# Optimization experiments

Measured on AMD Instinct MI355X. Metric: run time of the kernel, lower is better.

The kernel has to match this reference:

```python
import jax, jax.numpy as jnp
import numpy as np

B, Q, K, QSIZE, KSIZE, H, VDIM = 4, 1024, 1024, 256, 256, 32, 256


def setup_inputs() -> dict:
    key = jax.random.key(0)
    ks = jax.random.split(key, 10)
    return {
        "keys": jax.random.normal(ks[0], (B, K, KSIZE), dtype=jnp.float32),
        "queries": jax.random.normal(ks[1], (B, Q, QSIZE), dtype=jnp.float32),
        "values": jax.random.normal(ks[2], (B, K, VDIM), dtype=jnp.float32),
        "valid_lens": jax.random.randint(ks[3], (B,), 1, K + 1, dtype=jnp.int32),
        "W_q": jax.random.normal(ks[4], (QSIZE, H), dtype=jnp.float32) * (QSIZE ** -0.5),
        "b_q": jnp.zeros((H,), dtype=jnp.float32),
        "W_k": jax.random.normal(ks[5], (KSIZE, H), dtype=jnp.float32) * (KSIZE ** -0.5),
        "b_k": jnp.zeros((H,), dtype=jnp.float32),
        "w_v": jax.random.normal(ks[6], (H,), dtype=jnp.float32) * (H ** -0.5),
        "b_v": jnp.zeros((), dtype=jnp.float32),
    }


def reference(keys, queries, values, valid_lens, W_q, b_q, W_k, b_k, w_v, b_v):
    # projected features: (B,K,H) and (B,Q,H)
    fk = keys @ W_k + b_k
    fq = queries @ W_q + b_q
    # broadcast add -> (B,Q,K,H), tanh, then scalar projection -> scores (B,Q,K)
    features = jnp.tanh(fq[:, :, None, :] + fk[:, None, :, :])
    scores = jnp.einsum("bqkh,h->bqk", features, w_v) + b_v
    # masked softmax over key axis: positions >= valid_len get -1e6
    mask = jnp.arange(K)[None, None, :] < valid_lens[:, None, None]
    scores = jnp.where(mask, scores, jnp.float32(-1e6))
    weights = jax.nn.softmax(scores, axis=-1)
    # bmm: (B,Q,K) @ (B,K,V) -> (B,Q,V)
    return jnp.einsum("bqk,bkv->bqv", weights, values)
```

## Files before the change

kernel.cpp:

```cpp
#include <hip/hip_runtime.h>
#include <math.h>


#define NB 4
#define NQ 1024
#define NK 1024
#define DQK 256
#define NH 32
#define NV 256
#define TQ 8

__device__ __forceinline__ float fast_rcp(float x) { return __builtin_amdgcn_rcpf(x); }

__global__ __launch_bounds__(256) void proj_kernel(
    const float* __restrict__ queries, const float* __restrict__ keys,
    const float* __restrict__ W_q, const float* __restrict__ b_q,
    const float* __restrict__ W_k, const float* __restrict__ b_k,
    float* __restrict__ eq, float* __restrict__ ek)
{
    const int tid = blockIdx.x * 256 + threadIdx.x;
    const int h4  = (tid & 7) * 4;
    const int row = tid >> 3;

    const float* src; const float* W; const float* bias; float* dst; int r;
    if (row < NB * NQ) { r = row;            src = queries + (size_t)r * DQK; W = W_q; bias = b_q; dst = eq; }
    else               { r = row - NB * NQ;  src = keys    + (size_t)r * DQK; W = W_k; bias = b_k; dst = ek; }

    float4 bv4 = *(const float4*)(bias + h4);
    float a0 = bv4.x, a1 = bv4.y, a2 = bv4.z, a3 = bv4.w;
    #pragma unroll 4
    for (int i = 0; i < DQK; i += 4) {
        float4 s  = *(const float4*)(src + i);
        float4 w0 = *(const float4*)(W + (size_t)(i + 0) * NH + h4);
        float4 w1 = *(const float4*)(W + (size_t)(i + 1) * NH + h4);
        float4 w2 = *(const float4*)(W + (size_t)(i + 2) * NH + h4);
        float4 w3 = *(const float4*)(W + (size_t)(i + 3) * NH + h4);
        a0 = fmaf(s.x, w0.x, a0); a1 = fmaf(s.x, w0.y, a1); a2 = fmaf(s.x, w0.z, a2); a3 = fmaf(s.x, w0.w, a3);
        a0 = fmaf(s.y, w1.x, a0); a1 = fmaf(s.y, w1.y, a1); a2 = fmaf(s.y, w1.z, a2); a3 = fmaf(s.y, w1.w, a3);
        a0 = fmaf(s.z, w2.x, a0); a1 = fmaf(s.z, w2.y, a1); a2 = fmaf(s.z, w2.z, a2); a3 = fmaf(s.z, w2.w, a3);
        a0 = fmaf(s.w, w3.x, a0); a1 = fmaf(s.w, w3.y, a1); a2 = fmaf(s.w, w3.z, a2); a3 = fmaf(s.w, w3.w, a3);
    }
    float4 o;
    o.x = __expf(2.f * a0); o.y = __expf(2.f * a1);
    o.z = __expf(2.f * a2); o.w = __expf(2.f * a3);
    *(float4*)(dst + (size_t)r * NH + h4) = o;
}

__global__ __launch_bounds__(256) void attn_kernel(
    const float* __restrict__ eq, const float* __restrict__ ek,
    const float* __restrict__ values, const int* __restrict__ valid_lens,
    const float* __restrict__ w_v, float* __restrict__ out)
{
    __shared__ float s_w[NK][TQ];
    __shared__ float s_part[4][TQ];

    const int t    = threadIdx.x;
    const int b    = blockIdx.x >> 7;
    const int q0   = (blockIdx.x & 127) * TQ;
    const int nvalid = valid_lens[b];
    const int wave = t >> 6;
    const int lane = t & 63;
    const int qi   = t & 7;
    const int ks   = t >> 3;

    float wv[NH];
    #pragma unroll
    for (int h = 0; h < NH; h += 4) {
        float4 w4 = *(const float4*)(w_v + h);
        wv[h] = w4.x; wv[h+1] = w4.y; wv[h+2] = w4.z; wv[h+3] = w4.w;
    }
    float eqr[NH];
    const float* eqp = eq + (size_t)(b * NQ + q0 + qi) * NH;
    #pragma unroll
    for (int h = 0; h < NH; h += 4) {
        float4 e4 = *(const float4*)(eqp + h);
        eqr[h] = e4.x; eqr[h+1] = e4.y; eqr[h+2] = e4.z; eqr[h+3] = e4.w;
    }

    const float* ekbase = ek + (size_t)b * NK * NH;
    float ssum = 0.f;
    for (int i = 0; i < 32; i++) {
        const int k = ks + 32 * i;
        float e = 0.f;
        if (k < nvalid) {
            const float* ekp = ekbase + (size_t)k * NH;
            float acc = 0.f;
            #pragma unroll
            for (int h = 0; h < NH; h += 4) {
                float4 e4 = *(const float4*)(ekp + h);
                acc = fmaf(wv[h+0], fast_rcp(1.f + eqr[h+0] * e4.x), acc);
                acc = fmaf(wv[h+1], fast_rcp(1.f + eqr[h+1] * e4.y), acc);
                acc = fmaf(wv[h+2], fast_rcp(1.f + eqr[h+2] * e4.z), acc);
                acc = fmaf(wv[h+3], fast_rcp(1.f + eqr[h+3] * e4.w), acc);
            }
            e = __expf(-2.f * acc);
        }
        s_w[k][qi] = e;
        ssum += e;
    }

    ssum += __shfl_xor(ssum, 8, 64);
    ssum += __shfl_xor(ssum, 16, 64);
    ssum += __shfl_xor(ssum, 32, 64);
    if (lane < TQ) s_part[wave][lane] = ssum;
    __syncthreads();

    const int kpw  = (nvalid + 3) >> 2;
    const int kbeg = wave * kpw;
    const int kend = min(nvalid, kbeg + kpw);
    float4 acc0 = {0,0,0,0}, acc1 = {0,0,0,0}, acc2 = {0,0,0,0}, acc3 = {0,0,0,0};
    float4 acc4 = {0,0,0,0}, acc5 = {0,0,0,0}, acc6 = {0,0,0,0}, acc7 = {0,0,0,0};
    const float* vbase = values + (size_t)b * NK * NV + 4 * lane;

#define FMA4(A, W) A.x = fmaf((W), v.x, A.x); A.y = fmaf((W), v.y, A.y); \
                   A.z = fmaf((W), v.z, A.z); A.w = fmaf((W), v.w, A.w);
    #pragma unroll 2
    for (int k = kbeg; k < kend; k++) {
        float4 v  = *(const float4*)(vbase + (size_t)k * NV);
        float4 w0 = *(const float4*)(&s_w[k][0]);
        float4 w1 = *(const float4*)(&s_w[k][4]);
        FMA4(acc0, w0.x); FMA4(acc1, w0.y); FMA4(acc2, w0.z); FMA4(acc3, w0.w);
        FMA4(acc4, w1.x); FMA4(acc5, w1.y); FMA4(acc6, w1.z); FMA4(acc7, w1.w);
    }
#undef FMA4

    __syncthreads();
    float* sred = &s_w[0][0];
    {
        float4* p = (float4*)(sred + (size_t)(wave * TQ) * 256 + 4 * lane);
        p[0*64] = acc0; p[1*64] = acc1; p[2*64] = acc2; p[3*64] = acc3;
        p[4*64] = acc4; p[5*64] = acc5; p[6*64] = acc6; p[7*64] = acc7;
    }
    __syncthreads();

    float* obase = out + (size_t)(b * NQ + q0) * NV + t;
    #pragma unroll
    for (int q = 0; q < TQ; q++) {
        float tot = s_part[0][q] + s_part[1][q] + s_part[2][q] + s_part[3][q];
        float rs  = fast_rcp(tot);
        float r = sred[(0*TQ + q) * 256 + t] + sred[(1*TQ + q) * 256 + t]
                + sred[(2*TQ + q) * 256 + t] + sred[(3*TQ + q) * 256 + t];
        obase[(size_t)q * NV] = r * rs;
    }
}

extern "C" void kernel_launch(void* const* d_in, const int* in_sizes, int n_in,
                              void* d_out, int out_size, void* d_ws, size_t ws_size,
                              hipStream_t stream) {
    (void)in_sizes; (void)n_in; (void)out_size; (void)ws_size;
    const float* keys       = (const float*)d_in[0];
    const float* queries    = (const float*)d_in[1];
    const float* values     = (const float*)d_in[2];
    const int*   valid_lens = (const int*)d_in[3];
    const float* W_q        = (const float*)d_in[4];
    const float* b_q        = (const float*)d_in[5];
    const float* W_k        = (const float*)d_in[6];
    const float* b_k        = (const float*)d_in[7];
    const float* w_v        = (const float*)d_in[8];
    float* out = (float*)d_out;

    float* eq = (float*)d_ws;
    float* ek = eq + (size_t)NB * NQ * NH;

    proj_kernel<<<dim3(256), dim3(256), 0, stream>>>(queries, keys, W_q, b_q, W_k, b_k, eq, ek);
    attn_kernel<<<dim3(NB * (NQ / TQ)), dim3(256), 0, stream>>>(eq, ek, values, valid_lens, w_v, out);
}
```

Baseline: 123.8 us.

## Split projection reduction across lanes and double attention block to 512 threads

```diff
diff --git a/kernel.cpp b/kernel.cpp
--- a/kernel.cpp
+++ b/kernel.cpp
@@ -9,6 +9,7 @@
 #define NH 32
 #define NV 256
 #define TQ 8
+#define BLK 512
 
 __device__ __forceinline__ float fast_rcp(float x) { return __builtin_amdgcn_rcpf(x); }
 
@@ -18,18 +19,24 @@
     const float* __restrict__ W_k, const float* __restrict__ b_k,
     float* __restrict__ eq, float* __restrict__ ek)
 {
-    const int tid = blockIdx.x * 256 + threadIdx.x;
-    const int h4  = (tid & 7) * 4;
-    const int row = tid >> 3;
+    const int tid     = blockIdx.x * 256 + threadIdx.x;
+    const int row     = tid >> 5;
+    const int sub     = tid & 31;
+    const int h4      = (sub & 7) * 4;
+    const int quarter = sub >> 3;
 
     const float* src; const float* W; const float* bias; float* dst; int r;
-    if (row < NB * NQ) { r = row;            src = queries + (size_t)r * DQK; W = W_q; bias = b_q; dst = eq; }
-    else               { r = row - NB * NQ;  src = keys    + (size_t)r * DQK; W = W_k; bias = b_k; dst = ek; }
+    if (row < NB * NQ) { r = row;           src = queries + (size_t)r * DQK; W = W_q; bias = b_q; dst = eq; }
+    else               { r = row - NB * NQ; src = keys    + (size_t)r * DQK; W = W_k; bias = b_k; dst = ek; }
 
-    float4 bv4 = *(const float4*)(bias + h4);
-    float a0 = bv4.x, a1 = bv4.y, a2 = bv4.z, a3 = bv4.w;
+    float a0 = 0.f, a1 = 0.f, a2 = 0.f, a3 = 0.f;
+    if (quarter == 0) {
+        float4 bv4 = *(const float4*)(bias + h4);
+        a0 = bv4.x; a1 = bv4.y; a2 = bv4.z; a3 = bv4.w;
+    }
+    const int d0 = quarter * 64;
     #pragma unroll 4
-    for (int i = 0; i < DQK; i += 4) {
+    for (int i = d0; i < d0 + 64; i += 4) {
         float4 s  = *(const float4*)(src + i);
         float4 w0 = *(const float4*)(W + (size_t)(i + 0) * NH + h4);
         float4 w1 = *(const float4*)(W + (size_t)(i + 1) * NH + h4);
@@ -40,28 +47,34 @@
         a0 = fmaf(s.z, w2.x, a0); a1 = fmaf(s.z, w2.y, a1); a2 = fmaf(s.z, w2.z, a2); a3 = fmaf(s.z, w2.w, a3);
         a0 = fmaf(s.w, w3.x, a0); a1 = fmaf(s.w, w3.y, a1); a2 = fmaf(s.w, w3.z, a2); a3 = fmaf(s.w, w3.w, a3);
     }
-    float4 o;
-    o.x = __expf(2.f * a0); o.y = __expf(2.f * a1);
-    o.z = __expf(2.f * a2); o.w = __expf(2.f * a3);
-    *(float4*)(dst + (size_t)r * NH + h4) = o;
+    a0 += __shfl_xor(a0, 8, 64);  a1 += __shfl_xor(a1, 8, 64);
+    a2 += __shfl_xor(a2, 8, 64);  a3 += __shfl_xor(a3, 8, 64);
+    a0 += __shfl_xor(a0, 16, 64); a1 += __shfl_xor(a1, 16, 64);
+    a2 += __shfl_xor(a2, 16, 64); a3 += __shfl_xor(a3, 16, 64);
+    if (quarter == 0) {
+        float4 o;
+        o.x = __expf(2.f * a0); o.y = __expf(2.f * a1);
+        o.z = __expf(2.f * a2); o.w = __expf(2.f * a3);
+        *(float4*)(dst + (size_t)r * NH + h4) = o;
+    }
 }
 
-__global__ __launch_bounds__(256) void attn_kernel(
+__global__ __launch_bounds__(BLK) void attn_kernel(
     const float* __restrict__ eq, const float* __restrict__ ek,
     const float* __restrict__ values, const int* __restrict__ valid_lens,
     const float* __restrict__ w_v, float* __restrict__ out)
 {
     __shared__ float s_w[NK][TQ];
-    __shared__ float s_part[4][TQ];
+    __shared__ float s_part[8][TQ];
 
-    const int t    = threadIdx.x;
-    const int b    = blockIdx.x >> 7;
-    const int q0   = (blockIdx.x & 127) * TQ;
+    const int t      = threadIdx.x;
+    const int b      = blockIdx.x >> 7;
+    const int q0     = (blockIdx.x & 127) * TQ;
     const int nvalid = valid_lens[b];
-    const int wave = t >> 6;
-    const int lane = t & 63;
-    const int qi   = t & 7;
-    const int ks   = t >> 3;
+    const int wave   = t >> 6;
+    const int lane   = t & 63;
+    const int qi     = t & 7;
+    const int ks     = t >> 3;
 
     float wv[NH];
     #pragma unroll
@@ -78,9 +91,10 @@
     }
 
     const float* ekbase = ek + (size_t)b * NK * NH;
+    const int imax = (nvalid + 63) >> 6;
     float ssum = 0.f;
-    for (int i = 0; i < 32; i++) {
-        const int k = ks + 32 * i;
+    for (int i = 0; i < imax; i++) {
+        const int k = ks + 64 * i;
         float e = 0.f;
         if (k < nvalid) {
             const float* ekp = ekbase + (size_t)k * NH;
@@ -105,7 +119,7 @@
     if (lane < TQ) s_part[wave][lane] = ssum;
     __syncthreads();
 
-    const int kpw  = (nvalid + 3) >> 2;
+    const int kpw  = (nvalid + 7) >> 3;
     const int kbeg = wave * kpw;
     const int kend = min(nvalid, kbeg + kpw);
     float4 acc0 = {0,0,0,0}, acc1 = {0,0,0,0}, acc2 = {0,0,0,0}, acc3 = {0,0,0,0};
@@ -126,20 +140,33 @@
 
     __syncthreads();
     float* sred = &s_w[0][0];
-    {
-        float4* p = (float4*)(sred + (size_t)(wave * TQ) * 256 + 4 * lane);
+    float4* p = (float4*)(sred + (size_t)((wave & 3) * TQ) * 256) + lane;
+    if (wave < 4) {
         p[0*64] = acc0; p[1*64] = acc1; p[2*64] = acc2; p[3*64] = acc3;
         p[4*64] = acc4; p[5*64] = acc5; p[6*64] = acc6; p[7*64] = acc7;
     }
     __syncthreads();
+    if (wave >= 4) {
+        float4 x;
+#define ACC4(I, A) x = p[I*64]; x.x += A.x; x.y += A.y; x.z += A.z; x.w += A.w; p[I*64] = x;
+        ACC4(0, acc0); ACC4(1, acc1); ACC4(2, acc2); ACC4(3, acc3);
+        ACC4(4, acc4); ACC4(5, acc5); ACC4(6, acc6); ACC4(7, acc7);
+#undef ACC4
+    }
+    __syncthreads();
 
-    float* obase = out + (size_t)(b * NQ + q0) * NV + t;
+    const int v  = t & 255;
+    const int qh = (t >> 8) * 4;
+    float* obase = out + (size_t)(b * NQ + q0) * NV + v;
     #pragma unroll
-    for (int q = 0; q < TQ; q++) {
-        float tot = s_part[0][q] + s_part[1][q] + s_part[2][q] + s_part[3][q];
-        float rs  = fast_rcp(tot);
-        float r = sred[(0*TQ + q) * 256 + t] + sred[(1*TQ + q) * 256 + t]
-                + sred[(2*TQ + q) * 256 + t] + sred[(3*TQ + q) * 256 + t];
+    for (int j = 0; j < 4; j++) {
+        const int q = qh + j;
+        float tot = 0.f;
+        #pragma unroll
+        for (int w = 0; w < 8; w++) tot += s_part[w][q];
+        float rs = fast_rcp(tot);
+        float r = sred[(0*TQ + q) * 256 + v] + sred[(1*TQ + q) * 256 + v]
+                + sred[(2*TQ + q) * 256 + v] + sred[(3*TQ + q) * 256 + v];
         obase[(size_t)q * NV] = r * rs;
     }
 }
@@ -162,6 +189,6 @@
     float* eq = (float*)d_ws;
     float* ek = eq + (size_t)NB * NQ * NH;
 
-    proj_kernel<<<dim3(256), dim3(256), 0, stream>>>(queries, keys, W_q, b_q, W_k, b_k, eq, ek);
-    attn_kernel<<<dim3(NB * (NQ / TQ)), dim3(256), 0, stream>>>(eq, ek, values, valid_lens, w_v, out);
+    proj_kernel<<<dim3(1024), dim3(256), 0, stream>>>(queries, keys, W_q, b_q, W_k, b_k, eq, ek);
+    attn_kernel<<<dim3(NB * (NQ / TQ)), dim3(BLK), 0, stream>>>(eq, ek, values, valid_lens, w_v, out);
 }
```

After: 110.8 us. 1.12x faster.
